# Optimization experiments

Hardware: AMD Instinct MI355X
Metric: run time of the kernel (lower is better)

## Reference

```python
import jax, jax.numpy as jnp
import numpy as np

B_, N_, DIM, MDIM, H, HID = 8, 1024, 256, 128, 8, 1024
HD = DIM // H      # 32
MHD = MDIM // H    # 16
EPS = 1e-5


def _bn(x, g, b):
    # x: [B, C, L]; BatchNorm1d with batch statistics (training-mode fwd), biased var
    m = x.mean(axis=(0, 2), keepdims=True)
    v = x.var(axis=(0, 2), keepdims=True)
    return (x - m) / jnp.sqrt(v + EPS) * g[None, :, None] + b[None, :, None]


def setup_inputs() -> dict:
    key = jax.random.key(0)
    ks = jax.random.split(key, 12)
    p = lambda k, s: 0.02 * jax.random.normal(k, s, dtype=jnp.float32)
    z = lambda n: jnp.zeros((n,), jnp.float32)
    return {
        "x": jax.random.normal(ks[0], (B_, DIM, N_), dtype=jnp.float32),
        "cor": jax.random.uniform(ks[1], (B_, N_, 3), dtype=jnp.float32),
        "q_w": p(ks[2], (DIM, DIM)),            # qkv_bias=False
        "kv_w": p(ks[3], (2 * DIM, DIM)),
        "cor_w": p(ks[4], (MDIM, 3)),
        "proj_w": p(ks[5], (DIM, DIM)), "proj_b": z(DIM),
        "mproj_w": p(ks[6], (MDIM, MDIM)), "mproj_b": z(MDIM),
        "g1": jnp.ones((DIM,), jnp.float32), "b1": z(DIM),
        "g2": jnp.ones((DIM,), jnp.float32), "b2": z(DIM),
        "fc1_w": p(ks[7], (HID, DIM)), "fc1_b": z(HID),
        "dw_w": 1.0 + p(ks[8], (HID,)), "dw_b": z(HID),  # Conv1d k=1 groups=C -> per-channel affine
        "prelu_a": jnp.array(0.25, jnp.float32),
        "fc2_w": p(ks[9], (DIM, HID)), "fc2_b": z(DIM),
        "N": N_,
        "B": B_,
    }


def reference(x, cor, q_w, kv_w, cor_w, proj_w, proj_b, mproj_w, mproj_b,
              g1, b1, g2, b2, fc1_w, fc1_b, dw_w, dw_b, prelu_a,
              fc2_w, fc2_b, N, B):
    nwB = x.shape[0]
    scale = float(HD) ** -0.5
    # norm1 + to tokens [B, N, C]
    xn = _bn(x, g1, b1).transpose(0, 2, 1)
    # swap batch halves (frame reversal)
    xr = jnp.concatenate([xn[nwB // 2:], xn[:nwB // 2]], axis=0)
    # attention projections
    q = (xn @ q_w.T).reshape(nwB, N_, H, HD).transpose(0, 2, 1, 3)       # [B,H,N,hd]
    kv = (xr @ kv_w.T).reshape(nwB, N_, 2, H, HD).transpose(2, 0, 3, 1, 4)
    k, v = kv[0], kv[1]
    ce = cor @ cor_w.T                                                    # [B,N,M]
    ceh = ce.reshape(nwB, N_, H, MHD).transpose(0, 2, 1, 3)               # [B,H,N,mhd]
    attn = jax.nn.softmax(jnp.einsum('bhnd,bhmd->bhnm', q, k) * scale, axis=-1)
    # attention matrix reused for value and motion paths
    xa = (attn @ v).transpose(0, 2, 1, 3).reshape(nwB, N_, DIM) @ proj_w.T + proj_b
    cr = (attn @ ceh).transpose(0, 2, 1, 3).reshape(nwB, N_, MDIM)
    motion = (cr - ce) @ mproj_w.T + mproj_b
    # residual + norm2 + DWConv-MLP
    xn2 = xn + xa                                                         # [B,N,C]
    xb = _bn(xn2.transpose(0, 2, 1), g2, b2).transpose(0, 2, 1)           # [B,N,C]
    h = xb @ fc1_w.T + fc1_b
    h = h * dw_w + dw_b                                                   # depthwise 1x1 conv
    h = jnp.where(h >= 0, h, prelu_a * h)                                 # PReLU
    out = h @ fc2_w.T + fc2_b
    x_out = x + out.transpose(0, 2, 1)                                    # [B,C,N]
    return (x_out, motion)
```

## Files before the change

kernel.cpp:

```cpp
#include <hip/hip_runtime.h>
#include <hip/hip_bf16.h>
#include <math.h>

#define C_DIM 256
#define N_PTS 1024
#define H_N 8
#define MDIM_N 128
#define HID_N 1024
#define EPSV 1e-5f
#define R_TOT 8192
#define CN 262144

typedef __bf16 bf16x8 __attribute__((ext_vector_type(8)));
typedef __bf16 bf16x4 __attribute__((ext_vector_type(4)));
typedef float f32x4 __attribute__((ext_vector_type(4)));

#define QSCALE 0.25503482f

__device__ inline unsigned short bfu(float f) {
  union { __bf16 h; unsigned short u; } c;
  c.h = (__bf16)f;
  return c.u;
}

__global__ __launch_bounds__(256)
void prep_k(const float* __restrict__ s0, const float* __restrict__ s1,
            const float* __restrict__ s2, const float* __restrict__ s3,
            const float* __restrict__ s4, const float* __restrict__ s5,
            __bf16* d0, __bf16* d1, __bf16* d2, __bf16* d3, __bf16* d4,
            __bf16* d5, const float* __restrict__ cor,
            const float* __restrict__ cw, __bf16* __restrict__ vt,
            const float* __restrict__ x, const float* __restrict__ g1,
            const float* __restrict__ b1, float* __restrict__ st,
            float* __restrict__ raw2) {
  int blk = blockIdx.x;
  int t = threadIdx.x;
  if (blk < 784) {
    int i = blk * 256 + t;
    const float* s; __bf16* d; int off;
    if      (i <  16384) { s = s0; d = d0; off = 0; }
    else if (i <  49152) { s = s1; d = d1; off = 16384; }
    else if (i <  65536) { s = s2; d = d2; off = 49152; }
    else if (i <  69632) { s = s3; d = d3; off = 65536; }
    else if (i < 135168) { s = s4; d = d4; off = 69632; }
    else                 { s = s5; d = d5; off = 135168; }
    int j = i - off;
    float4 v = ((const float4*)s)[j];
    ushort4 u;
    u.x = bfu(v.x); u.y = bfu(v.y); u.z = bfu(v.z); u.w = bfu(v.w);
    ((ushort4*)d)[j] = u;
  } else if (blk < 1040) {
    __shared__ float cs[768];
    int j = blk - 784;
    int bh = j & 63, b = bh >> 3, h = bh & 7;
    int n0 = (j >> 6) * 256;
    for (int i = t; i < 768; i += 256)
      cs[i] = cor[(size_t)(b * N_PTS + n0) * 3 + i];
    __syncthreads();
    int md = t >> 4, ns = (t & 15) * 16;
    float w0 = cw[(h * 16 + md) * 3 + 0];
    float w1 = cw[(h * 16 + md) * 3 + 1];
    float w2 = cw[(h * 16 + md) * 3 + 2];
    __bf16* dst = &vt[((size_t)bh * 48 + 32 + md) * 1024 + n0 + ns];
#pragma unroll
    for (int g2 = 0; g2 < 4; ++g2) {
      ushort4 u;
      float v0 = cs[(ns + g2 * 4 + 0) * 3] * w0 + cs[(ns + g2 * 4 + 0) * 3 + 1] * w1 + cs[(ns + g2 * 4 + 0) * 3 + 2] * w2;
      float v1 = cs[(ns + g2 * 4 + 1) * 3] * w0 + cs[(ns + g2 * 4 + 1) * 3 + 1] * w1 + cs[(ns + g2 * 4 + 1) * 3 + 2] * w2;
      float v2 = cs[(ns + g2 * 4 + 2) * 3] * w0 + cs[(ns + g2 * 4 + 2) * 3 + 1] * w1 + cs[(ns + g2 * 4 + 2) * 3 + 2] * w2;
      float v3 = cs[(ns + g2 * 4 + 3) * 3] * w0 + cs[(ns + g2 * 4 + 3) * 3 + 1] * w1 + cs[(ns + g2 * 4 + 3) * 3 + 2] * w2;
      u.x = bfu(v0); u.y = bfu(v1); u.z = bfu(v2); u.w = bfu(v3);
      *(ushort4*)&dst[g2 * 4] = u;
    }
  } else {
    __shared__ float ss[256], sq[256];
    int c = blk - 1040;
    if (blk == 1040) { raw2[t] = 0.f; raw2[256 + t] = 0.f; }
    float s = 0.f, q = 0.f;
    for (int i = 0; i < 32; ++i) {
      int idx = t + i * 256;
      int b = idx >> 10, n = idx & 1023;
      float v = x[(size_t)b * CN + (size_t)c * N_PTS + n];
      s += v; q += v * v;
    }
    ss[t] = s; sq[t] = q;
    __syncthreads();
    for (int off = 128; off > 0; off >>= 1) {
      if (t < off) { ss[t] += ss[t + off]; sq[t] += sq[t + off]; }
      __syncthreads();
    }
    if (t == 0) {
      float mean = ss[0] * (1.f / 8192.f);
      float var  = sq[0] * (1.f / 8192.f) - mean * mean;
      float sc   = g1[c] * rsqrtf(var + EPSV);
      st[c]          = sc;
      st[C_DIM + c]  = b1[c] - mean * sc;
    }
  }
}

__global__ __launch_bounds__(256)
void norm1_t_k(const float* __restrict__ x, const float* __restrict__ st,
               __bf16* __restrict__ xnb) {
  __shared__ float tile[32][33];
  int c0 = blockIdx.x * 32, n0 = blockIdx.y * 32, b = blockIdx.z;
  int tx = threadIdx.x, ty = threadIdx.y;
#pragma unroll
  for (int k = 0; k < 4; ++k) {
    int ci = ty + k * 8;
    int c = c0 + ci;
    float v = x[(size_t)b * CN + (size_t)c * N_PTS + n0 + tx];
    tile[ci][tx] = v * st[c] + st[C_DIM + c];
  }
  __syncthreads();
#pragma unroll
  for (int k = 0; k < 4; ++k) {
    int ni = ty + k * 8;
    xnb[((size_t)(b * N_PTS + n0 + ni)) * C_DIM + c0 + tx] =
        (__bf16)tile[tx][ni];
  }
}

__global__ __launch_bounds__(512)
void attn_k(const __bf16* __restrict__ qb, const __bf16* __restrict__ kb,
            const __bf16* __restrict__ vt, const float* __restrict__ cor,
            const float* __restrict__ cw, __bf16* __restrict__ av,
            __bf16* __restrict__ dmc) {
  __shared__ __bf16 Vt[2][48][136];
  __shared__ __bf16 Pbuf[8][16][72];

  int bh = blockIdx.x; int b = bh >> 3, h = bh & 7;
  int t = threadIdx.x;
  int w = t >> 6, lane = t & 63;
  int l15 = lane & 15, g = lane >> 4;

  int nloc0 = blockIdx.y * 128 + w * 16;
  bf16x8 aq =
      *(const bf16x8*)&qb[((size_t)bh * N_PTS + nloc0 + l15) * 32 + g * 8];

  const __bf16* ksrc = kb + (size_t)bh * N_PTS * 32;
  const __bf16* vsrc = vt + (size_t)bh * 48 * N_PTS;
  int vdv = t >> 4, vkg = t & 15;

  float mrun = -1e30f, lrun = 0.f;
  f32x4 acco[3];
#pragma unroll
  for (int mt = 0; mt < 3; ++mt) acco[mt] = (f32x4){0.f, 0.f, 0.f, 0.f};

  *(uint4*)&Vt[0][vdv][vkg * 8] =
      *(const uint4*)&vsrc[(size_t)vdv * N_PTS + vkg * 8];
  if (t < 256)
    *(uint4*)&Vt[0][32 + vdv][vkg * 8] =
        *(const uint4*)&vsrc[(size_t)(32 + vdv) * N_PTS + vkg * 8];
  __syncthreads();

  for (int kt = 0; kt < 8; ++kt) {
    int cur = kt & 1, nxt = cur ^ 1;
    uint4 vregA, vregB;
    if (kt < 7) {
      int key1 = (kt + 1) * 128;
      vregA = *(const uint4*)&vsrc[(size_t)vdv * N_PTS + key1 + vkg * 8];
      if (t < 256)
        vregB =
            *(const uint4*)&vsrc[(size_t)(32 + vdv) * N_PTS + key1 + vkg * 8];
    }

    f32x4 sq[8];
    const __bf16* kbase = &ksrc[(size_t)(kt * 128 + l15) * 32 + g * 8];
    __builtin_amdgcn_s_setprio(1);
#pragma unroll
    for (int nt = 0; nt < 8; ++nt) {
      bf16x8 kf = *(const bf16x8*)(kbase + nt * 512);
      f32x4 z = (f32x4){0.f, 0.f, 0.f, 0.f};
      sq[nt] = __builtin_amdgcn_mfma_f32_16x16x32_bf16(kf, aq, z, 0, 0, 0);
    }
    __builtin_amdgcn_s_setprio(0);

    float m0 = fmaxf(fmaxf(sq[0][0], sq[0][1]), fmaxf(sq[0][2], sq[0][3]));
    float m1 = fmaxf(fmaxf(sq[1][0], sq[1][1]), fmaxf(sq[1][2], sq[1][3]));
    float m2 = fmaxf(fmaxf(sq[2][0], sq[2][1]), fmaxf(sq[2][2], sq[2][3]));
    float m3 = fmaxf(fmaxf(sq[3][0], sq[3][1]), fmaxf(sq[3][2], sq[3][3]));
    float m4 = fmaxf(fmaxf(sq[4][0], sq[4][1]), fmaxf(sq[4][2], sq[4][3]));
    float m5 = fmaxf(fmaxf(sq[5][0], sq[5][1]), fmaxf(sq[5][2], sq[5][3]));
    float m6 = fmaxf(fmaxf(sq[6][0], sq[6][1]), fmaxf(sq[6][2], sq[6][3]));
    float m7 = fmaxf(fmaxf(sq[7][0], sq[7][1]), fmaxf(sq[7][2], sq[7][3]));
    float tm = fmaxf(fmaxf(fmaxf(m0, m1), fmaxf(m2, m3)),
                     fmaxf(fmaxf(m4, m5), fmaxf(m6, m7)));
    tm = fmaxf(tm, __shfl_xor(tm, 16));
    tm = fmaxf(tm, __shfl_xor(tm, 32));
    if (__ballot(tm > mrun + 3.0f) != 0ull) {
      float nm = fmaxf(mrun, tm);
      float corr = exp2f(mrun - nm);
      mrun = nm;
      lrun *= corr;
#pragma unroll
      for (int mt = 0; mt < 3; ++mt)
#pragma unroll
        for (int r = 0; r < 4; ++r) acco[mt][r] *= corr;
    }
#pragma unroll
    for (int nt = 0; nt < 8; ++nt)
#pragma unroll
      for (int r = 0; r < 4; ++r) sq[nt][r] = exp2f(sq[nt][r] - mrun);
    float s0 = (sq[0][0] + sq[0][1]) + (sq[0][2] + sq[0][3]);
    float s1 = (sq[1][0] + sq[1][1]) + (sq[1][2] + sq[1][3]);
    float s2 = (sq[2][0] + sq[2][1]) + (sq[2][2] + sq[2][3]);
    float s3 = (sq[3][0] + sq[3][1]) + (sq[3][2] + sq[3][3]);
    float s4 = (sq[4][0] + sq[4][1]) + (sq[4][2] + sq[4][3]);
    float s5 = (sq[5][0] + sq[5][1]) + (sq[5][2] + sq[5][3]);
    float s6 = (sq[6][0] + sq[6][1]) + (sq[6][2] + sq[6][3]);
    float s7 = (sq[7][0] + sq[7][1]) + (sq[7][2] + sq[7][3]);
    float rs = ((s0 + s1) + (s2 + s3)) + ((s4 + s5) + (s6 + s7));
    rs += __shfl_xor(rs, 16);
    rs += __shfl_xor(rs, 32);
    lrun += rs;

#pragma unroll
    for (int half = 0; half < 2; ++half) {
#pragma unroll
      for (int nt2 = 0; nt2 < 4; ++nt2) {
        int nt = half * 4 + nt2;
        bf16x4 pk;
        pk[0] = (__bf16)sq[nt][0]; pk[1] = (__bf16)sq[nt][1];
        pk[2] = (__bf16)sq[nt][2]; pk[3] = (__bf16)sq[nt][3];
        *(bf16x4*)&Pbuf[w][l15][nt2 * 16 + g * 4] = pk;
      }
      bf16x8 ap0 = *(const bf16x8*)&Pbuf[w][l15][g * 8];
      bf16x8 ap1 = *(const bf16x8*)&Pbuf[w][l15][32 + g * 8];
      __builtin_amdgcn_s_setprio(1);
#pragma unroll
      for (int mt = 0; mt < 3; ++mt) {
        bf16x8 vf0 =
            *(const bf16x8*)&Vt[cur][mt * 16 + l15][half * 64 + g * 8];
        acco[mt] =
            __builtin_amdgcn_mfma_f32_16x16x32_bf16(vf0, ap0, acco[mt], 0, 0, 0);
        bf16x8 vf1 =
            *(const bf16x8*)&Vt[cur][mt * 16 + l15][half * 64 + 32 + g * 8];
        acco[mt] =
            __builtin_amdgcn_mfma_f32_16x16x32_bf16(vf1, ap1, acco[mt], 0, 0, 0);
      }
      __builtin_amdgcn_s_setprio(0);
    }

    if (kt < 7) {
      *(uint4*)&Vt[nxt][vdv][vkg * 8] = vregA;
      if (t < 256) *(uint4*)&Vt[nxt][32 + vdv][vkg * 8] = vregB;
      __syncthreads();
    }
  }

  float inv = 1.f / lrun;
  int row = b * N_PTS + nloc0 + l15;
#pragma unroll
  for (int mt = 0; mt < 2; ++mt) {
    ushort4 o;
    o.x = bfu(acco[mt][0] * inv); o.y = bfu(acco[mt][1] * inv);
    o.z = bfu(acco[mt][2] * inv); o.w = bfu(acco[mt][3] * inv);
    *(ushort4*)&av[(size_t)row * C_DIM + h * 32 + mt * 16 + g * 4] = o;
  }
  {
    const float* cp = &cor[(size_t)row * 3];
    float c0 = cp[0], c1 = cp[1], c2 = cp[2];
    ushort4 o;
#pragma unroll
    for (int r = 0; r < 4; ++r) {
      int md = h * 16 + g * 4 + r;
      float ce = c0 * cw[md * 3] + c1 * cw[md * 3 + 1] + c2 * cw[md * 3 + 2];
      float v = acco[2][r] * inv - ce;
      ((unsigned short*)&o)[r] = bfu(v);
    }
    *(ushort4*)&dmc[(size_t)row * MDIM_N + h * 16 + g * 4] = o;
  }
}

template <int MODE, int BMt, int BNt>
__global__ __launch_bounds__(256)
void mgemm_k(const __bf16* __restrict__ A, const __bf16* __restrict__ W,
             const float* __restrict__ bias, void* __restrict__ outp,
             const float* __restrict__ e0, __bf16* __restrict__ kbp,
             __bf16* __restrict__ vtp, int K, int M) {
  constexpr int WRW = BMt / 2;
  constexpr int MF = WRW / 16;
  constexpr int WN = BNt / 2;
  constexpr int NR = WN / 16;
  constexpr int APASS = BMt / 32;
  constexpr int BPASS = BNt / 32;
  __shared__ __bf16 Al[BMt * 64];
  __shared__ __bf16 Bl[BNt * 64];
  int t = threadIdx.x;
  int w = t >> 6, lane = t & 63;
  int l15 = lane & 15, g = lane >> 4;
  int wr = w >> 1, wn = w & 1;
  int r0 = blockIdx.y * BMt;
  int m0 = blockIdx.x * BNt;
  bool swapA = (MODE == 1) && (m0 >= 256);

  f32x4 acc[MF][NR];
#pragma unroll
  for (int i = 0; i < MF; ++i)
#pragma unroll
    for (int j = 0; j < NR; ++j) acc[i][j] = (f32x4){0.f, 0.f, 0.f, 0.f};

  for (int kt = 0; kt < K; kt += 64) {
    __syncthreads();
#pragma unroll
    for (int p = 0; p < APASS; ++p) {
      int flat = p * 256 + t;
      int row = flat >> 3, c16 = flat & 7;
      int gr = r0 + row;
      if (swapA) gr = ((((gr >> 10) + 4) & 7) << 10) | (gr & 1023);
      *(uint4*)&Al[row * 64 + (c16 ^ (row & 7)) * 8] =
          *(const uint4*)&A[(size_t)gr * K + kt + c16 * 8];
    }
#pragma unroll
    for (int p = 0; p < BPASS; ++p) {
      int flat = p * 256 + t;
      int row = flat >> 3, c16 = flat & 7;
      *(uint4*)&Bl[row * 64 + (c16 ^ (row & 7)) * 8] =
          *(const uint4*)&W[(size_t)(m0 + row) * K + kt + c16 * 8];
    }
    __syncthreads();
#pragma unroll
    for (int ks = 0; ks < 2; ++ks) {
      bf16x8 af[MF], bf_[NR];
#pragma unroll
      for (int mf = 0; mf < MF; ++mf) {
        int row = wr * WRW + mf * 16 + l15;
        af[mf] = *(const bf16x8*)&Al[row * 64 + ((ks * 4 + g) ^ (l15 & 7)) * 8];
      }
#pragma unroll
      for (int nf = 0; nf < NR; ++nf) {
        int row = wn * WN + nf * 16 + l15;
        bf_[nf] = *(const bf16x8*)&Bl[row * 64 + ((ks * 4 + g) ^ (l15 & 7)) * 8];
      }
#pragma unroll
      for (int mf = 0; mf < MF; ++mf)
#pragma unroll
        for (int nf = 0; nf < NR; ++nf)
          acc[mf][nf] = __builtin_amdgcn_mfma_f32_16x16x32_bf16(
              af[mf], bf_[nf], acc[mf][nf], 0, 0, 0);
    }
  }

#pragma unroll
  for (int mf = 0; mf < MF; ++mf) {
#pragma unroll
    for (int nf = 0; nf < NR; ++nf) {
      int m = m0 + wn * WN + nf * 16 + l15;
      int rbase = r0 + wr * WRW + mf * 16 + g * 4;
      if (MODE == 5) {
        int b = rbase >> 10, n = rbase & 1023;
        size_t oi = (size_t)b * CN + (size_t)m * N_PTS + n;
        float4 xv = *(const float4*)&e0[oi];
        float bs = bias[m];
        float4 ov;
        ov.x = xv.x + acc[mf][nf][0] + bs;
        ov.y = xv.y + acc[mf][nf][1] + bs;
        ov.z = xv.z + acc[mf][nf][2] + bs;
        ov.w = xv.w + acc[mf][nf][3] + bs;
        *(float4*)&((float*)outp)[oi] = ov;
      } else if (MODE == 1 && m0 >= 512) {
        int d = m - 512, hh = d >> 5, dd = d & 31;
        int b = rbase >> 10, n0v = rbase & 1023;
        ushort4 uu;
        uu.x = bfu(acc[mf][nf][0]); uu.y = bfu(acc[mf][nf][1]);
        uu.z = bfu(acc[mf][nf][2]); uu.w = bfu(acc[mf][nf][3]);
        *(ushort4*)&vtp[(((size_t)b * 8 + hh) * 48 + dd) * 1024 + n0v] = uu;
      } else {
#pragma unroll
        for (int r = 0; r < 4; ++r) {
          float v = acc[mf][nf][r];
          int b = rbase >> 10, n = (rbase & 1023) + r;
          if (m0 < 256) {
            int hh = m >> 5, dd = m & 31;
            ((__bf16*)outp)[(((size_t)b * 8 + hh) * 1024 + n) * 32 + dd] =
                (__bf16)(v * QSCALE);
          } else {
            int d = m - 256, hh = d >> 5, dd = d & 31;
            kbp[(((size_t)b * 8 + hh) * 1024 + n) * 32 + dd] = (__bf16)v;
          }
        }
      }
    }
  }
}

__global__ __launch_bounds__(256)
void projmot_k(const __bf16* __restrict__ av, const __bf16* __restrict__ pw,
               const float* __restrict__ pb, __bf16* __restrict__ xn2b,
               const __bf16* __restrict__ xnb, const __bf16* __restrict__ dmc,
               const __bf16* __restrict__ mw, const float* __restrict__ mb,
               float* __restrict__ mot, float* __restrict__ raw2) {
  __shared__ __bf16 Al[64 * 64];
  __shared__ __bf16 Bl[64 * 64];
  bool isProj = blockIdx.x < 4;
  const __bf16* A = isProj ? av : dmc;
  const __bf16* W = isProj ? pw : mw;
  const float* bias = isProj ? pb : mb;
  int K = isProj ? 256 : 128;
  int m0 = (isProj ? blockIdx.x : (blockIdx.x - 4)) * 64;
  int t = threadIdx.x;
  int w = t >> 6, lane = t & 63;
  int l15 = lane & 15, g = lane >> 4;
  int wr = w >> 1, wn = w & 1;
  int r0 = blockIdx.y * 64;

  f32x4 acc[2][2];
#pragma unroll
  for (int i = 0; i < 2; ++i)
#pragma unroll
    for (int j = 0; j < 2; ++j) acc[i][j] = (f32x4){0.f, 0.f, 0.f, 0.f};

  for (int kt = 0; kt < K; kt += 64) {
    __syncthreads();
#pragma unroll
    for (int p = 0; p < 2; ++p) {
      int flat = p * 256 + t;
      int row = flat >> 3, c16 = flat & 7;
      *(uint4*)&Al[row * 64 + (c16 ^ (row & 7)) * 8] =
          *(const uint4*)&A[(size_t)(r0 + row) * K + kt + c16 * 8];
    }
#pragma unroll
    for (int p = 0; p < 2; ++p) {
      int flat = p * 256 + t;
      int row = flat >> 3, c16 = flat & 7;
      *(uint4*)&Bl[row * 64 + (c16 ^ (row & 7)) * 8] =
          *(const uint4*)&W[(size_t)(m0 + row) * K + kt + c16 * 8];
    }
    __syncthreads();
#pragma unroll
    for (int ks = 0; ks < 2; ++ks) {
      bf16x8 af[2], bf_[2];
#pragma unroll
      for (int mf = 0; mf < 2; ++mf) {
        int row = wr * 32 + mf * 16 + l15;
        af[mf] = *(const bf16x8*)&Al[row * 64 + ((ks * 4 + g) ^ (l15 & 7)) * 8];
      }
#pragma unroll
      for (int nf = 0; nf < 2; ++nf) {
        int row = wn * 32 + nf * 16 + l15;
        bf_[nf] = *(const bf16x8*)&Bl[row * 64 + ((ks * 4 + g) ^ (l15 & 7)) * 8];
      }
#pragma unroll
      for (int mf = 0; mf < 2; ++mf)
#pragma unroll
        for (int nf = 0; nf < 2; ++nf)
          acc[mf][nf] = __builtin_amdgcn_mfma_f32_16x16x32_bf16(
              af[mf], bf_[nf], acc[mf][nf], 0, 0, 0);
    }
  }

  float sS[2] = {0.f, 0.f}, sQ[2] = {0.f, 0.f};
#pragma unroll
  for (int mf = 0; mf < 2; ++mf) {
#pragma unroll
    for (int nf = 0; nf < 2; ++nf) {
      int m = m0 + wn * 32 + nf * 16 + l15;
      int rbase = r0 + wr * 32 + mf * 16 + g * 4;
#pragma unroll
      for (int r = 0; r < 4; ++r) {
        float v = acc[mf][nf][r];
        if (isProj) {
          size_t oi = (size_t)(rbase + r) * C_DIM + m;
          float vv = (float)xnb[oi] + v + bias[m];
          xn2b[oi] = (__bf16)vv;
          sS[nf] += vv;
          sQ[nf] += vv * vv;
        } else {
          mot[(size_t)(rbase + r) * MDIM_N + m] = v + bias[m];
        }
      }
    }
  }

  if (isProj) {
    __syncthreads();
    float* colS = (float*)&Al[0];
    float* colQ = colS + 64;
    if (t < 128) colS[t] = 0.f;
    __syncthreads();
#pragma unroll
    for (int nf = 0; nf < 2; ++nf) {
      int mc = wn * 32 + nf * 16 + l15;
      atomicAdd(&colS[mc], sS[nf]);
      atomicAdd(&colQ[mc], sQ[nf]);
    }
    __syncthreads();
    if (t < 64) {
      atomicAdd(&raw2[m0 + t], colS[t]);
      atomicAdd(&raw2[256 + m0 + t], colQ[t]);
    }
  }
}

__global__ __launch_bounds__(256)
void fc1_k(const __bf16* __restrict__ xn2b, const float* __restrict__ raw2,
           const float* __restrict__ g2, const float* __restrict__ b2,
           const __bf16* __restrict__ W, const float* __restrict__ bias,
           const float* __restrict__ dw_w, const float* __restrict__ dw_b,
           const float* __restrict__ pre, __bf16* __restrict__ hb) {
  __shared__ __bf16 Al[64 * 64];
  __shared__ __bf16 Bl[128 * 64];
  __shared__ float scs[256], shs[256];
  int t = threadIdx.x;
  int w = t >> 6, lane = t & 63;
  int l15 = lane & 15, g = lane >> 4;
  int wr = w >> 1, wn = w & 1;
  int r0 = blockIdx.y * 64;
  int m0 = blockIdx.x * 128;

  {
    float mean = raw2[t] * (1.f / 8192.f);
    float var  = raw2[256 + t] * (1.f / 8192.f) - mean * mean;
    float sc   = g2[t] * rsqrtf(var + EPSV);
    scs[t] = sc;
    shs[t] = b2[t] - mean * sc;
  }
  __syncthreads();

  f32x4 acc[2][4];
#pragma unroll
  for (int i = 0; i < 2; ++i)
#pragma unroll
    for (int j = 0; j < 4; ++j) acc[i][j] = (f32x4){0.f, 0.f, 0.f, 0.f};

  for (int kt = 0; kt < 256; kt += 64) {
    __syncthreads();
#pragma unroll
    for (int p = 0; p < 2; ++p) {
      int flat = p * 256 + t;
      int row = flat >> 3, c16 = flat & 7;
      int k = kt + c16 * 8;
      bf16x8 v8 = *(const bf16x8*)&xn2b[(size_t)(r0 + row) * C_DIM + k];
      bf16x8 a;
#pragma unroll
      for (int i = 0; i < 8; ++i)
        a[i] = (__bf16)((float)v8[i] * scs[k + i] + shs[k + i]);
      *(bf16x8*)&Al[row * 64 + (c16 ^ (row & 7)) * 8] = a;
    }
#pragma unroll
    for (int p = 0; p < 4; ++p) {
      int flat = p * 256 + t;
      int row = flat >> 3, c16 = flat & 7;
      *(uint4*)&Bl[row * 64 + (c16 ^ (row & 7)) * 8] =
          *(const uint4*)&W[(size_t)(m0 + row) * 256 + kt + c16 * 8];
    }
    __syncthreads();
#pragma unroll
    for (int ks = 0; ks < 2; ++ks) {
      bf16x8 af[2], bf_[4];
#pragma unroll
      for (int mf = 0; mf < 2; ++mf) {
        int row = wr * 32 + mf * 16 + l15;
        af[mf] = *(const bf16x8*)&Al[row * 64 + ((ks * 4 + g) ^ (l15 & 7)) * 8];
      }
#pragma unroll
      for (int nf = 0; nf < 4; ++nf) {
        int row = wn * 64 + nf * 16 + l15;
        bf_[nf] = *(const bf16x8*)&Bl[row * 64 + ((ks * 4 + g) ^ (l15 & 7)) * 8];
      }
#pragma unroll
      for (int mf = 0; mf < 2; ++mf)
#pragma unroll
        for (int nf = 0; nf < 4; ++nf)
          acc[mf][nf] = __builtin_amdgcn_mfma_f32_16x16x32_bf16(
              af[mf], bf_[nf], acc[mf][nf], 0, 0, 0);
    }
  }

  float a_pre = pre[0];
#pragma unroll
  for (int mf = 0; mf < 2; ++mf) {
#pragma unroll
    for (int nf = 0; nf < 4; ++nf) {
      int m = m0 + wn * 64 + nf * 16 + l15;
      int rbase = r0 + wr * 32 + mf * 16 + g * 4;
      float bs = bias[m], dwm = dw_w[m], dbm = dw_b[m];
#pragma unroll
      for (int r = 0; r < 4; ++r) {
        float v = acc[mf][nf][r] + bs;
        v = v * dwm + dbm;
        hb[(size_t)(rbase + r) * HID_N + m] =
            (__bf16)(v >= 0.f ? v : a_pre * v);
      }
    }
  }
}

extern "C" void kernel_launch(void* const* d_in, const int* in_sizes, int n_in,
                              void* d_out, int out_size, void* d_ws,
                              size_t ws_size, hipStream_t stream) {
  const float* x       = (const float*)d_in[0];
  const float* cor     = (const float*)d_in[1];
  const float* q_w     = (const float*)d_in[2];
  const float* kv_w    = (const float*)d_in[3];
  const float* cor_w   = (const float*)d_in[4];
  const float* proj_w  = (const float*)d_in[5];
  const float* proj_b  = (const float*)d_in[6];
  const float* mproj_w = (const float*)d_in[7];
  const float* mproj_b = (const float*)d_in[8];
  const float* g1      = (const float*)d_in[9];
  const float* b1      = (const float*)d_in[10];
  const float* g2      = (const float*)d_in[11];
  const float* b2      = (const float*)d_in[12];
  const float* fc1_w   = (const float*)d_in[13];
  const float* fc1_b   = (const float*)d_in[14];
  const float* dw_w    = (const float*)d_in[15];
  const float* dw_b    = (const float*)d_in[16];
  const float* prelu   = (const float*)d_in[17];
  const float* fc2_w   = (const float*)d_in[18];
  const float* fc2_b   = (const float*)d_in[19];

  char* base = (char*)d_ws;
  const size_t MB = 1u << 20;
  __bf16* xnb  = (__bf16*)(base + 8 * MB);
  __bf16* qb   = (__bf16*)(base + 12 * MB);
  __bf16* kb   = (__bf16*)(base + 16 * MB);
  __bf16* vt   = (__bf16*)(base + 20 * MB);
  __bf16* av   = (__bf16*)(base + 30 * MB);
  __bf16* dmc  = (__bf16*)(base + 34 * MB);
  __bf16* xn2b = (__bf16*)(base + 36 * MB);
  __bf16* hb   = (__bf16*)(base + 12 * MB);
  __bf16* qwb  = (__bf16*)(base + 44 * MB);
  __bf16* kvwb = (__bf16*)(base + 44 * MB + 131072);
  __bf16* pwb  = (__bf16*)(base + 44 * MB + 393216);
  __bf16* mwb  = (__bf16*)(base + 44 * MB + 524288);
  __bf16* f1wb = (__bf16*)(base + 44 * MB + 557056);
  __bf16* f2wb = (__bf16*)(base + 44 * MB + 1081344);
  float*  raw2 = (float*)(base + 45 * MB + 655360);
  float*  st1  = raw2 + 1024;
  float* out0 = (float*)d_out;
  float* out1 = out0 + 2097152;

  prep_k<<<1296, 256, 0, stream>>>(q_w, kv_w, proj_w, mproj_w, fc1_w, fc2_w,
                                   qwb, kvwb, pwb, mwb, f1wb, f2wb,
                                   cor, cor_w, vt, x, g1, b1, st1, raw2);
  norm1_t_k<<<dim3(8, 32, 8), dim3(32, 8), 0, stream>>>(x, st1, xnb);

  mgemm_k<1, 64, 128><<<dim3(6, 128), 256, 0, stream>>>(
      xnb, qwb, nullptr, qb, nullptr, kb, vt, 256, 768);

  attn_k<<<dim3(64, 8), 512, 0, stream>>>(qb, kb, vt, cor, cor_w, av, dmc);

  projmot_k<<<dim3(6, 128), 256, 0, stream>>>(av, pwb, proj_b, xn2b, xnb,
                                              dmc, mwb, mproj_b, out1, raw2);

  fc1_k<<<dim3(8, 128), 256, 0, stream>>>(xn2b, raw2, g2, b2, f1wb, fc1_b,
                                          dw_w, dw_b, prelu, hb);

  mgemm_k<5, 64, 64><<<dim3(4, 128), 256, 0, stream>>>(
      hb, f2wb, fc2_b, out0, x, nullptr, nullptr, HID_N, 256);
}
```

Before: 97.08 us.

## Fuse norm1 transpose into QKV GEMM and recompute xn in projection epilogue

```diff
diff --git a/kernel.cpp b/kernel.cpp
--- a/kernel.cpp
+++ b/kernel.cpp
@@ -100,24 +100,106 @@
 }
 
 __global__ __launch_bounds__(256)
-void norm1_t_k(const float* __restrict__ x, const float* __restrict__ st,
-               __bf16* __restrict__ xnb) {
-  __shared__ float tile[32][33];
-  int c0 = blockIdx.x * 32, n0 = blockIdx.y * 32, b = blockIdx.z;
-  int tx = threadIdx.x, ty = threadIdx.y;
-#pragma unroll
-  for (int k = 0; k < 4; ++k) {
-    int ci = ty + k * 8;
-    int c = c0 + ci;
-    float v = x[(size_t)b * CN + (size_t)c * N_PTS + n0 + tx];
-    tile[ci][tx] = v * st[c] + st[C_DIM + c];
-  }
-  __syncthreads();
-#pragma unroll
-  for (int k = 0; k < 4; ++k) {
-    int ni = ty + k * 8;
-    xnb[((size_t)(b * N_PTS + n0 + ni)) * C_DIM + c0 + tx] =
-        (__bf16)tile[tx][ni];
+void qkv_k(const float* __restrict__ x, const float* __restrict__ st,
+           const __bf16* __restrict__ W, __bf16* __restrict__ qbp,
+           __bf16* __restrict__ kbp, __bf16* __restrict__ vtp) {
+  __shared__ __bf16 Al[64 * 64];
+  __shared__ __bf16 Bl[128 * 64];
+  int t = threadIdx.x;
+  int w = t >> 6, lane = t & 63;
+  int l15 = lane & 15, g = lane >> 4;
+  int wr = w >> 1, wn = w & 1;
+  int r0 = blockIdx.y * 64;
+  int m0 = blockIdx.x * 128;
+  int b0 = r0 >> 10, n0 = r0 & 1023;
+  int ab = (m0 >= 256) ? ((b0 + 4) & 7) : b0;
+
+  int cl = t >> 2;
+  int jb = (t & 3) * 16;
+
+  f32x4 acc[2][4];
+#pragma unroll
+  for (int i = 0; i < 2; ++i)
+#pragma unroll
+    for (int j = 0; j < 4; ++j) acc[i][j] = (f32x4){0.f, 0.f, 0.f, 0.f};
+
+  for (int kt = 0; kt < 256; kt += 64) {
+    __syncthreads();
+    {
+      int c = kt + cl;
+      float sc = st[c], sh = st[C_DIM + c];
+      const float* xrow = &x[((size_t)ab * C_DIM + c) * N_PTS + n0 + jb];
+      int sw = ((cl >> 3) << 3);
+#pragma unroll
+      for (int i = 0; i < 4; ++i) {
+        float4 v = *(const float4*)(xrow + 4 * i);
+#pragma unroll
+        for (int e = 0; e < 4; ++e) {
+          int nl = jb + 4 * i + e;
+          float vv = ((const float*)&v)[e] * sc + sh;
+          Al[nl * 64 + (sw ^ ((nl & 7) << 3)) + (cl & 7)] = (__bf16)vv;
+        }
+      }
+    }
+#pragma unroll
+    for (int p = 0; p < 4; ++p) {
+      int flat = p * 256 + t;
+      int row = flat >> 3, c16 = flat & 7;
+      *(uint4*)&Bl[row * 64 + (c16 ^ (row & 7)) * 8] =
+          *(const uint4*)&W[(size_t)(m0 + row) * 256 + kt + c16 * 8];
+    }
+    __syncthreads();
+#pragma unroll
+    for (int ks = 0; ks < 2; ++ks) {
+      bf16x8 af[2], bf_[4];
+#pragma unroll
+      for (int mf = 0; mf < 2; ++mf) {
+        int row = wr * 32 + mf * 16 + l15;
+        af[mf] = *(const bf16x8*)&Al[row * 64 + ((ks * 4 + g) ^ (l15 & 7)) * 8];
+      }
+#pragma unroll
+      for (int nf = 0; nf < 4; ++nf) {
+        int row = wn * 64 + nf * 16 + l15;
+        bf_[nf] = *(const bf16x8*)&Bl[row * 64 + ((ks * 4 + g) ^ (l15 & 7)) * 8];
+      }
+#pragma unroll
+      for (int mf = 0; mf < 2; ++mf)
+#pragma unroll
+        for (int nf = 0; nf < 4; ++nf)
+          acc[mf][nf] = __builtin_amdgcn_mfma_f32_16x16x32_bf16(
+              af[mf], bf_[nf], acc[mf][nf], 0, 0, 0);
+    }
+  }
+
+#pragma unroll
+  for (int mf = 0; mf < 2; ++mf) {
+#pragma unroll
+    for (int nf = 0; nf < 4; ++nf) {
+      int m = m0 + wn * 64 + nf * 16 + l15;
+      int rbase = r0 + wr * 32 + mf * 16 + g * 4;
+      if (m0 >= 512) {
+        int d = m - 512, hh = d >> 5, dd = d & 31;
+        int b = rbase >> 10, n0v = rbase & 1023;
+        ushort4 uu;
+        uu.x = bfu(acc[mf][nf][0]); uu.y = bfu(acc[mf][nf][1]);
+        uu.z = bfu(acc[mf][nf][2]); uu.w = bfu(acc[mf][nf][3]);
+        *(ushort4*)&vtp[(((size_t)b * 8 + hh) * 48 + dd) * 1024 + n0v] = uu;
+      } else {
+#pragma unroll
+        for (int r = 0; r < 4; ++r) {
+          float v = acc[mf][nf][r];
+          int b = rbase >> 10, n = (rbase & 1023) + r;
+          if (m < 256) {
+            int hh = m >> 5, dd = m & 31;
+            qbp[(((size_t)b * 8 + hh) * 1024 + n) * 32 + dd] =
+                (__bf16)(v * QSCALE);
+          } else {
+            int d = m - 256, hh = d >> 5, dd = d & 31;
+            kbp[(((size_t)b * 8 + hh) * 1024 + n) * 32 + dd] = (__bf16)v;
+          }
+        }
+      }
+    }
   }
 }
 
@@ -273,124 +355,13 @@
   }
 }
 
-template <int MODE, int BMt, int BNt>
-__global__ __launch_bounds__(256)
-void mgemm_k(const __bf16* __restrict__ A, const __bf16* __restrict__ W,
-             const float* __restrict__ bias, void* __restrict__ outp,
-             const float* __restrict__ e0, __bf16* __restrict__ kbp,
-             __bf16* __restrict__ vtp, int K, int M) {
-  constexpr int WRW = BMt / 2;
-  constexpr int MF = WRW / 16;
-  constexpr int WN = BNt / 2;
-  constexpr int NR = WN / 16;
-  constexpr int APASS = BMt / 32;
-  constexpr int BPASS = BNt / 32;
-  __shared__ __bf16 Al[BMt * 64];
-  __shared__ __bf16 Bl[BNt * 64];
-  int t = threadIdx.x;
-  int w = t >> 6, lane = t & 63;
-  int l15 = lane & 15, g = lane >> 4;
-  int wr = w >> 1, wn = w & 1;
-  int r0 = blockIdx.y * BMt;
-  int m0 = blockIdx.x * BNt;
-  bool swapA = (MODE == 1) && (m0 >= 256);
-
-  f32x4 acc[MF][NR];
-#pragma unroll
-  for (int i = 0; i < MF; ++i)
-#pragma unroll
-    for (int j = 0; j < NR; ++j) acc[i][j] = (f32x4){0.f, 0.f, 0.f, 0.f};
-
-  for (int kt = 0; kt < K; kt += 64) {
-    __syncthreads();
-#pragma unroll
-    for (int p = 0; p < APASS; ++p) {
-      int flat = p * 256 + t;
-      int row = flat >> 3, c16 = flat & 7;
-      int gr = r0 + row;
-      if (swapA) gr = ((((gr >> 10) + 4) & 7) << 10) | (gr & 1023);
-      *(uint4*)&Al[row * 64 + (c16 ^ (row & 7)) * 8] =
-          *(const uint4*)&A[(size_t)gr * K + kt + c16 * 8];
-    }
-#pragma unroll
-    for (int p = 0; p < BPASS; ++p) {
-      int flat = p * 256 + t;
-      int row = flat >> 3, c16 = flat & 7;
-      *(uint4*)&Bl[row * 64 + (c16 ^ (row & 7)) * 8] =
-          *(const uint4*)&W[(size_t)(m0 + row) * K + kt + c16 * 8];
-    }
-    __syncthreads();
-#pragma unroll
-    for (int ks = 0; ks < 2; ++ks) {
-      bf16x8 af[MF], bf_[NR];
-#pragma unroll
-      for (int mf = 0; mf < MF; ++mf) {
-        int row = wr * WRW + mf * 16 + l15;
-        af[mf] = *(const bf16x8*)&Al[row * 64 + ((ks * 4 + g) ^ (l15 & 7)) * 8];
-      }
-#pragma unroll
-      for (int nf = 0; nf < NR; ++nf) {
-        int row = wn * WN + nf * 16 + l15;
-        bf_[nf] = *(const bf16x8*)&Bl[row * 64 + ((ks * 4 + g) ^ (l15 & 7)) * 8];
-      }
-#pragma unroll
-      for (int mf = 0; mf < MF; ++mf)
-#pragma unroll
-        for (int nf = 0; nf < NR; ++nf)
-          acc[mf][nf] = __builtin_amdgcn_mfma_f32_16x16x32_bf16(
-              af[mf], bf_[nf], acc[mf][nf], 0, 0, 0);
-    }
-  }
-
-#pragma unroll
-  for (int mf = 0; mf < MF; ++mf) {
-#pragma unroll
-    for (int nf = 0; nf < NR; ++nf) {
-      int m = m0 + wn * WN + nf * 16 + l15;
-      int rbase = r0 + wr * WRW + mf * 16 + g * 4;
-      if (MODE == 5) {
-        int b = rbase >> 10, n = rbase & 1023;
-        size_t oi = (size_t)b * CN + (size_t)m * N_PTS + n;
-        float4 xv = *(const float4*)&e0[oi];
-        float bs = bias[m];
-        float4 ov;
-        ov.x = xv.x + acc[mf][nf][0] + bs;
-        ov.y = xv.y + acc[mf][nf][1] + bs;
-        ov.z = xv.z + acc[mf][nf][2] + bs;
-        ov.w = xv.w + acc[mf][nf][3] + bs;
-        *(float4*)&((float*)outp)[oi] = ov;
-      } else if (MODE == 1 && m0 >= 512) {
-        int d = m - 512, hh = d >> 5, dd = d & 31;
-        int b = rbase >> 10, n0v = rbase & 1023;
-        ushort4 uu;
-        uu.x = bfu(acc[mf][nf][0]); uu.y = bfu(acc[mf][nf][1]);
-        uu.z = bfu(acc[mf][nf][2]); uu.w = bfu(acc[mf][nf][3]);
-        *(ushort4*)&vtp[(((size_t)b * 8 + hh) * 48 + dd) * 1024 + n0v] = uu;
-      } else {
-#pragma unroll
-        for (int r = 0; r < 4; ++r) {
-          float v = acc[mf][nf][r];
-          int b = rbase >> 10, n = (rbase & 1023) + r;
-          if (m0 < 256) {
-            int hh = m >> 5, dd = m & 31;
-            ((__bf16*)outp)[(((size_t)b * 8 + hh) * 1024 + n) * 32 + dd] =
-                (__bf16)(v * QSCALE);
-          } else {
-            int d = m - 256, hh = d >> 5, dd = d & 31;
-            kbp[(((size_t)b * 8 + hh) * 1024 + n) * 32 + dd] = (__bf16)v;
-          }
-        }
-      }
-    }
-  }
-}
-
 __global__ __launch_bounds__(256)
 void projmot_k(const __bf16* __restrict__ av, const __bf16* __restrict__ pw,
                const float* __restrict__ pb, __bf16* __restrict__ xn2b,
-               const __bf16* __restrict__ xnb, const __bf16* __restrict__ dmc,
-               const __bf16* __restrict__ mw, const float* __restrict__ mb,
-               float* __restrict__ mot, float* __restrict__ raw2) {
+               const float* __restrict__ x, const float* __restrict__ st1,
+               const __bf16* __restrict__ dmc, const __bf16* __restrict__ mw,
+               const float* __restrict__ mb, float* __restrict__ mot,
+               float* __restrict__ raw2) {
   __shared__ __bf16 Al[64 * 64];
   __shared__ __bf16 Bl[64 * 64];
   bool isProj = blockIdx.x < 4;
@@ -457,18 +428,22 @@
     for (int nf = 0; nf < 2; ++nf) {
       int m = m0 + wn * 32 + nf * 16 + l15;
       int rbase = r0 + wr * 32 + mf * 16 + g * 4;
-#pragma unroll
-      for (int r = 0; r < 4; ++r) {
-        float v = acc[mf][nf][r];
-        if (isProj) {
-          size_t oi = (size_t)(rbase + r) * C_DIM + m;
-          float vv = (float)xnb[oi] + v + bias[m];
-          xn2b[oi] = (__bf16)vv;
+      if (isProj) {
+        int b = rbase >> 10, n = rbase & 1023;
+        float4 xv = *(const float4*)&x[((size_t)b * C_DIM + m) * N_PTS + n];
+        float sc = st1[m], sh = st1[C_DIM + m];
+        float bs = bias[m];
+#pragma unroll
+        for (int r = 0; r < 4; ++r) {
+          float vv = ((const float*)&xv)[r] * sc + sh + acc[mf][nf][r] + bs;
+          xn2b[(size_t)(rbase + r) * C_DIM + m] = (__bf16)vv;
           sS[nf] += vv;
           sQ[nf] += vv * vv;
-        } else {
-          mot[(size_t)(rbase + r) * MDIM_N + m] = v + bias[m];
         }
+      } else {
+#pragma unroll
+        for (int r = 0; r < 4; ++r)
+          mot[(size_t)(rbase + r) * MDIM_N + m] = acc[mf][nf][r] + bias[m];
       }
     }
   }
@@ -583,6 +558,84 @@
         hb[(size_t)(rbase + r) * HID_N + m] =
             (__bf16)(v >= 0.f ? v : a_pre * v);
       }
+    }
+  }
+}
+
+__global__ __launch_bounds__(256)
+void fc2_k(const __bf16* __restrict__ A, const __bf16* __restrict__ W,
+           const float* __restrict__ bias, float* __restrict__ outp,
+           const float* __restrict__ e0) {
+  __shared__ __bf16 Al[64 * 64];
+  __shared__ __bf16 Bl[64 * 64];
+  int t = threadIdx.x;
+  int w = t >> 6, lane = t & 63;
+  int l15 = lane & 15, g = lane >> 4;
+  int wr = w >> 1, wn = w & 1;
+  int r0 = blockIdx.y * 64;
+  int m0 = blockIdx.x * 64;
+
+  f32x4 acc[2][2];
+#pragma unroll
+  for (int i = 0; i < 2; ++i)
+#pragma unroll
+    for (int j = 0; j < 2; ++j) acc[i][j] = (f32x4){0.f, 0.f, 0.f, 0.f};
+
+  for (int kt = 0; kt < 1024; kt += 64) {
+    __syncthreads();
+#pragma unroll
+    for (int p = 0; p < 2; ++p) {
+      int flat = p * 256 + t;
+      int row = flat >> 3, c16 = flat & 7;
+      *(uint4*)&Al[row * 64 + (c16 ^ (row & 7)) * 8] =
+          *(const uint4*)&A[(size_t)(r0 + row) * 1024 + kt + c16 * 8];
+    }
+#pragma unroll
+    for (int p = 0; p < 2; ++p) {
+      int flat = p * 256 + t;
+      int row = flat >> 3, c16 = flat & 7;
+      *(uint4*)&Bl[row * 64 + (c16 ^ (row & 7)) * 8] =
+          *(const uint4*)&W[(size_t)(m0 + row) * 1024 + kt + c16 * 8];
+    }
+    __syncthreads();
+#pragma unroll
+    for (int ks = 0; ks < 2; ++ks) {
+      bf16x8 af[2], bf_[2];
+#pragma unroll
+      for (int mf = 0; mf < 2; ++mf) {
+        int row = wr * 32 + mf * 16 + l15;
+        af[mf] = *(const bf16x8*)&Al[row * 64 + ((ks * 4 + g) ^ (l15 & 7)) * 8];
+      }
+#pragma unroll
+      for (int nf = 0; nf < 2; ++nf) {
+        int row = wn * 32 + nf * 16 + l15;
+        bf_[nf] = *(const bf16x8*)&Bl[row * 64 + ((ks * 4 + g) ^ (l15 & 7)) * 8];
+      }
+#pragma unroll
+      for (int mf = 0; mf < 2; ++mf)
+#pragma unroll
+        for (int nf = 0; nf < 2; ++nf)
+          acc[mf][nf] = __builtin_amdgcn_mfma_f32_16x16x32_bf16(
+              af[mf], bf_[nf], acc[mf][nf], 0, 0, 0);
+    }
+  }
+
+#pragma unroll
+  for (int mf = 0; mf < 2; ++mf) {
+#pragma unroll
+    for (int nf = 0; nf < 2; ++nf) {
+      int m = m0 + wn * 32 + nf * 16 + l15;
+      int rbase = r0 + wr * 32 + mf * 16 + g * 4;
+      int b = rbase >> 10, n = rbase & 1023;
+      size_t oi = (size_t)b * CN + (size_t)m * N_PTS + n;
+      float4 xv = *(const float4*)&e0[oi];
+      float bs = bias[m];
+      float4 ov;
+      ov.x = xv.x + acc[mf][nf][0] + bs;
+      ov.y = xv.y + acc[mf][nf][1] + bs;
+      ov.z = xv.z + acc[mf][nf][2] + bs;
+      ov.w = xv.w + acc[mf][nf][3] + bs;
+      *(float4*)&outp[oi] = ov;
     }
   }
 }
@@ -613,7 +666,6 @@
 
   char* base = (char*)d_ws;
   const size_t MB = 1u << 20;
-  __bf16* xnb  = (__bf16*)(base + 8 * MB);
   __bf16* qb   = (__bf16*)(base + 12 * MB);
   __bf16* kb   = (__bf16*)(base + 16 * MB);
   __bf16* vt   = (__bf16*)(base + 20 * MB);
@@ -635,19 +687,16 @@
   prep_k<<<1296, 256, 0, stream>>>(q_w, kv_w, proj_w, mproj_w, fc1_w, fc2_w,
                                    qwb, kvwb, pwb, mwb, f1wb, f2wb,
                                    cor, cor_w, vt, x, g1, b1, st1, raw2);
-  norm1_t_k<<<dim3(8, 32, 8), dim3(32, 8), 0, stream>>>(x, st1, xnb);
-
-  mgemm_k<1, 64, 128><<<dim3(6, 128), 256, 0, stream>>>(
-      xnb, qwb, nullptr, qb, nullptr, kb, vt, 256, 768);
+
+  qkv_k<<<dim3(6, 128), 256, 0, stream>>>(x, st1, qwb, qb, kb, vt);
 
   attn_k<<<dim3(64, 8), 512, 0, stream>>>(qb, kb, vt, cor, cor_w, av, dmc);
 
-  projmot_k<<<dim3(6, 128), 256, 0, stream>>>(av, pwb, proj_b, xn2b, xnb,
+  projmot_k<<<dim3(6, 128), 256, 0, stream>>>(av, pwb, proj_b, xn2b, x, st1,
                                               dmc, mwb, mproj_b, out1, raw2);
 
   fc1_k<<<dim3(8, 128), 256, 0, stream>>>(xn2b, raw2, g2, b2, f1wb, fc1_b,
                                           dw_w, dw_b, prelu, hb);
 
-  mgemm_k<5, 64, 64><<<dim3(4, 128), 256, 0, stream>>>(
-      hb, f2wb, fc2_b, out0, x, nullptr, nullptr, HID_N, 256);
+  fc2_k<<<dim3(4, 128), 256, 0, stream>>>(hb, f2wb, fc2_b, out0, x);
 }
```

New measurement: 105.3 us. 8.4% more time.
